# Kernel tuning notes

Measured on AMD Instinct MI355X. Metric: run time of the kernel, lower is better.

Reference implementation:

```python
import jax, jax.numpy as jnp
import numpy as np

EPS = 1e-6

def setup_inputs() -> dict:
    key = jax.random.key(0)
    M, N, D = 6, 4096, 512
    output = jax.random.normal(key, (M, N, D), dtype=jnp.float32)
    return {"output": output}

def reference(output):
    # output: [M, N, D] stacked per-layer features (already flatten(1)'d)
    M, N, _ = output.shape
    # Gram matrices K_i = X_i @ X_i^T with zeroed diagonal: [M, N, N]
    K = jnp.einsum('ind,imd->inm', output, output)
    K = K * (1.0 - jnp.eye(N, dtype=K.dtype))
    # Double centering H@K@H == K - rowmean - colmean + totalmean
    row = jnp.mean(K, axis=2, keepdims=True)
    col = jnp.mean(K, axis=1, keepdims=True)
    tot = jnp.mean(K, axis=(1, 2), keepdims=True)
    Khat = K - row - col + tot
    # Pairwise HSIC(K_i, K_j) = |sum(Khat_i * Khat_j)| : [M, M]
    S = jnp.abs(jnp.einsum('inm,jnm->ij', Khat, Khat))
    diag = jnp.diagonal(S)
    cka = S / jnp.sqrt(diag[:, None] * diag[None, :] + EPS)
    # Original only fills the strict lower triangle
    hsic_matrix = cka * jnp.tril(jnp.ones((M, M), dtype=cka.dtype), k=-1)
    l = jnp.sum(jnp.abs(hsic_matrix))
    hsic_visual = hsic_matrix + hsic_matrix.T + jnp.eye(M, dtype=cka.dtype)
    return (hsic_visual, l)
```

## Files before the change

### kernel.cpp

```cpp
#include <hip/hip_runtime.h>
#include <hip/hip_bf16.h>
#include <stdint.h>


#define NPTS  4096
#define DF    512
#define ML    6
#define NPAIR 21
#define BKB   128
#define NDIAGBLK 60
#define NOFFBLK  240
#define NGEMMBLK (NDIAGBLK + NOFFBLK)
#define NSTATS   192
#define NTAIL    21
#define TILEB (128 * BKB)

typedef float  f32x4 __attribute__((ext_vector_type(4)));
typedef int    i32x4v __attribute__((ext_vector_type(4)));
typedef int    i32x8v __attribute__((ext_vector_type(8)));
typedef unsigned char u8;

__constant__ int c_PI[NPAIR] = {0,0,0,0,0,0, 1,1,1,1,1, 2,2,2,2, 3,3,3, 4,4, 5};
__constant__ int c_PJ[NPAIR] = {0,1,2,3,4,5, 1,2,3,4,5, 2,3,4,5, 3,4,5, 4,5, 5};
__constant__ int c_DIAGP[ML]  = {0, 6, 11, 15, 18, 20};
__constant__ int c_OFFP[15]   = {1,2,3,4,5, 7,8,9,10, 12,13,14, 16,17, 19};
__constant__ int c_TM[10] = {0,0,0,0, 1,1,1, 2,2, 3};
__constant__ int c_TN[10] = {0,1,2,3, 1,2,3, 2,3, 3};

#define OFF_XT8  0u
#define OFF_SP   12582912u
#define OFF_DVP  13369344u
#define OFF_F    14155776u
#define OFF_D    (OFF_F + 1024u)
#define OFF_XS   (OFF_D + 98304u)
#define OFF_DD   (OFF_XS + 98304u)
#define OFF_RD   (OFF_DD + 256u)
#define OFF_T    (OFF_RD + 256u)

#define UNIT_SCALE 127

__device__ __forceinline__ unsigned short f2fp8x2(float a, float b) {
    return (unsigned short)(__builtin_amdgcn_cvt_pk_fp8_f32(a, b, 0, false) & 0xffff);
}

__device__ __forceinline__ void gl2lds16(const void* g, void* l) {
    __builtin_amdgcn_global_load_lds(
        (__attribute__((address_space(1))) void*)g,
        (__attribute__((address_space(3))) void*)l, 16, 0, 0);
}

__device__ __forceinline__ i32x8v frag32(const u8* base, int row, int quad) {
    int sw = row & 7;
    i32x4v lo = *(const i32x4v*)&base[row * BKB + ((2 * quad) ^ sw) * 16];
    i32x4v hi = *(const i32x4v*)&base[row * BKB + ((2 * quad + 1) ^ sw) * 16];
    return __builtin_shufflevector(lo, hi, 0, 1, 2, 3, 4, 5, 6, 7);
}

__device__ __forceinline__ void stage128(const u8* __restrict__ G, u8* L,
                                         int wave, int rl, int g, int k0) {
#pragma unroll
    for (int is = 0; is < 4; ++is) {
        int rbase = is * 32 + wave * 8;
        int r = rbase + rl;
        int gs = g ^ (r & 7);
        gl2lds16(G + (size_t)r * NPTS + k0 + gs * 16, &L[rbase * BKB]);
    }
}

__global__ __launch_bounds__(256) void k_transpose(const float* __restrict__ X,
                                                   u8* __restrict__ Xt8,
                                                   float* __restrict__ sp,
                                                   float* __restrict__ dvp,
                                                   float* __restrict__ F,
                                                   unsigned* __restrict__ cnt,
                                                   float* __restrict__ tbss,
                                                   float* __restrict__ dv,
                                                   float* __restrict__ xs) {
    __shared__ float tT[64][67];
    int nt = blockIdx.x, dt = blockIdx.y, l = blockIdx.z;
    int n0 = nt * 64, d0 = dt * 64;
    int t = threadIdx.x, q = t & 15, r = t >> 4;
    if (dt == 0) {
        int zb = (l << 6) + nt;
        if (t < 64)            dv[zb * 64 + t] = 0.f;
        else if (t < 128)      xs[zb * 64 + (t - 64)] = 0.f;
        if (zb == 0) {
            if (t >= 128 && t < 128 + NPAIR) F[t - 128] = 0.f;
            if (t == 155) *cnt = 0u;
            if (t >= 160 && t < 160 + ML) tbss[t - 160] = 0.f;
        }
    }
    const float4* src = (const float4*)(X + ((size_t)l * NPTS + n0) * DF + d0);
#pragma unroll
    for (int p = 0; p < 4; ++p) {
        int rr = r + 16 * p;
        float4 v = src[(size_t)rr * (DF / 4) + q];
        tT[4 * q + 0][rr] = v.x;
        tT[4 * q + 1][rr] = v.y;
        tT[4 * q + 2][rr] = v.z;
        tT[4 * q + 3][rr] = v.w;
    }
    __syncthreads();
    if (t < 64) {
        float cs = 0.f;
#pragma unroll
        for (int k = 0; k < 64; ++k) {
            int n = (6 * t + k) & 63;
            cs += tT[t][n];
        }
        sp[((l << 6) + nt) * DF + d0 + t] = cs;
    } else if (t < 128) {
        int n = t - 64;
        float rs = 0.f;
#pragma unroll
        for (int d = 0; d < 64; ++d) { float v = tT[d][n]; rs += v * v; }
        dvp[((l << 3) + dt) * NPTS + n0 + n] = rs;
    }
    int dcol = t >> 2, nb = (t & 3) * 16;
    uint4 o;
#pragma unroll
    for (int w2 = 0; w2 < 4; ++w2) {
        int j = nb + w2 * 4;
        unsigned lo = f2fp8x2(tT[dcol][j + 0], tT[dcol][j + 1]);
        unsigned hi = f2fp8x2(tT[dcol][j + 2], tT[dcol][j + 3]);
        ((unsigned*)&o)[w2] = lo | (hi << 16);
    }
    *(uint4*)(Xt8 + ((size_t)(l * DF + d0 + dcol)) * NPTS + n0 + nb) = o;
}

__global__ __launch_bounds__(256, 2) void k_gemm_frob(const u8* __restrict__ Xt8,
                                                      float* __restrict__ F,
                                                      const float* __restrict__ sp,
                                                      const float* __restrict__ dvp,
                                                      float* __restrict__ dv,
                                                      float* __restrict__ xs,
                                                      float* __restrict__ tbss) {
    __shared__ __align__(16) u8 As[2][TILEB];
    __shared__ __align__(16) u8 Bs[2][TILEB];

    int orig = blockIdx.x;
    int b = orig;
    if (orig < NGEMMBLK) {
        int xcd = orig & 7, idx = orig >> 3;
        const int q = NGEMMBLK >> 3, r = NGEMMBLK & 7;
        b = (xcd < r ? xcd * (q + 1) : r * (q + 1) + (xcd - r) * q) + idx;
    }
    int t = threadIdx.x, wave = t >> 6, lane = t & 63;
    int rl = lane >> 3, g = lane & 7;
    int row16 = lane & 15, quad = lane >> 4;

    if (b < NGEMMBLK) {
        const u8* A;
        const u8* B;
        int p;
        float w = 1.0f;
        if (b < NDIAGBLK) {
            int li = b / 10, tt = b % 10;
            p = c_DIAGP[li];
            w = (c_TM[tt] == c_TN[tt]) ? 1.0f : 2.0f;
            A = Xt8 + ((size_t)(li * DF + c_TM[tt] * 128)) * NPTS;
            B = Xt8 + ((size_t)(li * DF + c_TN[tt] * 128)) * NPTS;
        } else {
            int b2 = b - NDIAGBLK, op = b2 >> 4, tile = b2 & 15;
            p = c_OFFP[op];
            A = Xt8 + ((size_t)(c_PI[p] * DF + (tile & 3) * 128)) * NPTS;
            B = Xt8 + ((size_t)(c_PJ[p] * DF + (tile >> 2) * 128)) * NPTS;
        }

        int wr = (wave >> 1) * 64, wc = (wave & 1) * 64;
        f32x4 acc[4][4];
#pragma unroll
        for (int mi = 0; mi < 4; ++mi)
#pragma unroll
            for (int ni = 0; ni < 4; ++ni) acc[mi][ni] = (f32x4)0.0f;

        stage128(A, As[0], wave, rl, g, 0);
        stage128(B, Bs[0], wave, rl, g, 0);
        int cur = 0;
        const int NIT = NPTS / BKB;
        for (int it = 0; it < NIT; ++it) {
            if (it < NIT - 1) {
                int kN = (it + 1) * BKB;
                stage128(A, As[cur ^ 1], wave, rl, g, kN);
                stage128(B, Bs[cur ^ 1], wave, rl, g, kN);
                asm volatile("s_waitcnt vmcnt(8)" ::: "memory");
            } else {
                asm volatile("s_waitcnt vmcnt(0)" ::: "memory");
            }
            __builtin_amdgcn_s_barrier();
            asm volatile("" ::: "memory");
            i32x8v af[4];
#pragma unroll
            for (int mi = 0; mi < 4; ++mi)
                af[mi] = frag32(As[cur], wr + mi * 16 + row16, quad);
#pragma unroll
            for (int ni = 0; ni < 4; ++ni) {
                i32x8v bf = frag32(Bs[cur], wc + ni * 16 + row16, quad);
#pragma unroll
                for (int mi = 0; mi < 4; ++mi)
                    acc[mi][ni] = __builtin_amdgcn_mfma_scale_f32_16x16x128_f8f6f4(
                        af[mi], bf, acc[mi][ni], 0, 0,
                        0, UNIT_SCALE, 0, UNIT_SCALE);
            }
            asm volatile("s_waitcnt lgkmcnt(0)" ::: "memory");
            __builtin_amdgcn_s_barrier();
            asm volatile("" ::: "memory");
            cur ^= 1;
        }

        float local = 0.f;
#pragma unroll
        for (int mi = 0; mi < 4; ++mi)
#pragma unroll
            for (int ni = 0; ni < 4; ++ni)
#pragma unroll
                for (int e = 0; e < 4; ++e)
                    local += acc[mi][ni][e] * acc[mi][ni][e];
        for (int off = 32; off; off >>= 1) local += __shfl_down(local, off);
        __shared__ float wsum[4];
        if (lane == 0) wsum[wave] = local;
        __syncthreads();
        if (t == 0)
            atomicAdd(&F[p], w * (wsum[0] + wsum[1] + wsum[2] + wsum[3]));
    } else {
        int sid = b - NGEMMBLK;
        int l = sid >> 5, rem = sid & 31, dc = rem >> 2, nc = rem & 3;
        int d0 = dc * 64, n0 = nc * 1024;
        float* scratch = (float*)As;
        float* slp = (float*)As + 256;

        int dl = t & 63, part = t >> 6;
        float a = 0.f;
#pragma unroll 4
        for (int k = 0; k < 16; ++k)
            a += sp[((l << 6) + part * 16 + k) * DF + d0 + dl];
        scratch[t] = a;
        __syncthreads();
        if (t < 64)
            slp[t] = scratch[t] + scratch[64 + t] + scratch[128 + t] + scratch[192 + t];
        __syncthreads();
        if (nc == 0 && t == 0) {
            float q2 = 0.f;
#pragma unroll
            for (int d = 0; d < 64; ++d) q2 += slp[d] * slp[d];
            atomicAdd(&tbss[l], q2);
        }
        int n = n0 + t * 4;
        const u8* xb = Xt8 + (size_t)(l * DF + d0) * NPTS + n;
        float a0 = 0, a1 = 0, a2 = 0, a3 = 0;
#pragma unroll 8
        for (int dd = 0; dd < 64; ++dd) {
            unsigned v = *(const unsigned*)(xb + (size_t)dd * NPTS);
            float sv = slp[dd];
            a0 += sv * __builtin_amdgcn_cvt_f32_fp8(v, 0);
            a1 += sv * __builtin_amdgcn_cvt_f32_fp8(v, 1);
            a2 += sv * __builtin_amdgcn_cvt_f32_fp8(v, 2);
            a3 += sv * __builtin_amdgcn_cvt_f32_fp8(v, 3);
        }
        float* xo = xs + l * NPTS + n;
        atomicAdd(&xo[0], a0); atomicAdd(&xo[1], a1);
        atomicAdd(&xo[2], a2); atomicAdd(&xo[3], a3);
        float4 dp = *(const float4*)(dvp + ((l << 3) + dc) * NPTS + n);
        float* dvo = dv + l * NPTS + n;
        atomicAdd(&dvo[0], dp.x); atomicAdd(&dvo[1], dp.y);
        atomicAdd(&dvo[2], dp.z); atomicAdd(&dvo[3], dp.w);
    }
}

__global__ __launch_bounds__(256) void k_tail(const float* __restrict__ dv,
                                              const float* __restrict__ xs,
                                              const float* __restrict__ tbss,
                                              float* __restrict__ F,
                                              float* __restrict__ ddot,
                                              float* __restrict__ rdot,
                                              float* __restrict__ tb,
                                              unsigned* __restrict__ cnt,
                                              float* __restrict__ out) {
    __shared__ float4 red[256];
    __shared__ int lastFlag;
    __shared__ float tbv[ML];
    __shared__ double hs[ML][ML];
    __shared__ float cka[ML][ML];

    int b = blockIdx.x, t = threadIdx.x;

    {
        int p = b, i = c_PI[p], j = c_PJ[p];
        const float invN = 1.0f / (float)NPTS;
        float dd = 0.f, rr = 0.f, sd = 0.f;
        for (int n = t; n < NPTS; n += 256) {
            float di = dv[i * NPTS + n], dj = dv[j * NPTS + n];
            float ri = (xs[i * NPTS + n] - di) * invN;
            float rj = (xs[j * NPTS + n] - dj) * invN;
            dd += di * dj;
            rr += ri * rj;
            sd += di;
        }
        red[t] = make_float4(dd, rr, sd, 0.f);
        __syncthreads();
        for (int h = 128; h > 0; h >>= 1) {
            if (t < h) {
                float4 a = red[t], bb = red[t + h];
                red[t] = make_float4(a.x + bb.x, a.y + bb.y, a.z + bb.z, 0.f);
            }
            __syncthreads();
        }
        if (t == 0) {
            atomicExch(&ddot[p], red[0].x);
            atomicExch(&rdot[p], red[0].y);
            if (i == j)
                atomicExch(&tb[i],
                    (tbss[i] - red[0].z) * (1.0f / ((float)NPTS * (float)NPTS)));
        }
    }

    __syncthreads();
    if (t == 0) {
        __threadfence();
        unsigned old = atomicAdd(cnt, 1u);
        lastFlag = (old == NTAIL - 1);
    }
    __syncthreads();
    if (!lastFlag) return;
    __threadfence();
    if (t < ML) tbv[t] = atomicAdd(&tb[t], 0.0f);
    __syncthreads();
    if (t < NPAIR) {
        int i = c_PI[t], j = c_PJ[t];
        double Fv = (double)atomicAdd(&F[t], 0.0f);
        double dd = (double)atomicAdd(&ddot[t], 0.0f);
        double rd = (double)atomicAdd(&rdot[t], 0.0f);
        double v = Fv - dd - 2.0 * (double)NPTS * rd
                 + (double)NPTS * (double)NPTS * (double)tbv[i] * (double)tbv[j];
        hs[i][j] = v; hs[j][i] = v;
    }
    __syncthreads();
    if (t < ML * ML) {
        int i = t / ML, j = t % ML;
        float v;
        if (i == j) v = 1.0f;
        else v = (float)(fabs(hs[i][j]) / sqrt(hs[i][i] * hs[j][j] + 1e-6));
        cka[i][j] = v;
        out[t] = v;
    }
    __syncthreads();
    if (t == 0) {
        float l = 0.f;
        for (int i = 1; i < ML; ++i)
            for (int j = 0; j < i; ++j) l += cka[i][j];
        out[ML * ML] = l;
    }
}

extern "C" void kernel_launch(void* const* d_in, const int* in_sizes, int n_in,
                              void* d_out, int out_size, void* d_ws, size_t ws_size,
                              hipStream_t stream) {
    (void)in_sizes; (void)n_in; (void)out_size; (void)ws_size;
    const float* X = (const float*)d_in[0];
    float* out = (float*)d_out;
    char* ws = (char*)d_ws;
    u8*    Xt8 = (u8*)(ws + OFF_XT8);
    float* sp  = (float*)(ws + OFF_SP);
    float* dvp = (float*)(ws + OFF_DVP);
    float* F   = (float*)(ws + OFF_F);
    unsigned* cnt = (unsigned*)(ws + OFF_F + 256u);
    float* tbss = (float*)(ws + OFF_F + 512u);
    float* dv  = (float*)(ws + OFF_D);
    float* xs  = (float*)(ws + OFF_XS);
    float* dd  = (float*)(ws + OFF_DD);
    float* rd  = (float*)(ws + OFF_RD);
    float* tb  = (float*)(ws + OFF_T);

    hipLaunchKernelGGL(k_transpose, dim3(64, 8, 6), dim3(256), 0, stream,
                       X, Xt8, sp, dvp, F, cnt, tbss, dv, xs);
    hipLaunchKernelGGL(k_gemm_frob, dim3(NGEMMBLK + NSTATS), dim3(256), 0, stream,
                       Xt8, F, sp, dvp, dv, xs, tbss);
    hipLaunchKernelGGL(k_tail, dim3(NTAIL), dim3(256), 0, stream,
                       dv, xs, tbss, F, dd, rd, tb, cnt, out);
}
```

Before: 130.1 us.

## Use 512-thread blocks with 8 waves per GEMM tile and merge stats blocks

```diff
diff --git a/kernel.cpp b/kernel.cpp
--- a/kernel.cpp
+++ b/kernel.cpp
@@ -11,7 +11,7 @@
 #define NDIAGBLK 60
 #define NOFFBLK  240
 #define NGEMMBLK (NDIAGBLK + NOFFBLK)
-#define NSTATS   192
+#define NSTATS   96
 #define NTAIL    21
 #define TILEB (128 * BKB)
 
@@ -56,11 +56,11 @@
     return __builtin_shufflevector(lo, hi, 0, 1, 2, 3, 4, 5, 6, 7);
 }
 
-__device__ __forceinline__ void stage128(const u8* __restrict__ G, u8* L,
-                                         int wave, int rl, int g, int k0) {
-#pragma unroll
-    for (int is = 0; is < 4; ++is) {
-        int rbase = is * 32 + wave * 8;
+__device__ __forceinline__ void stage128w8(const u8* __restrict__ G, u8* L,
+                                           int wave, int rl, int g, int k0) {
+#pragma unroll
+    for (int is = 0; is < 2; ++is) {
+        int rbase = is * 64 + wave * 8;
         int r = rbase + rl;
         int gs = g ^ (r & 7);
         gl2lds16(G + (size_t)r * NPTS + k0 + gs * 16, &L[rbase * BKB]);
@@ -128,7 +128,7 @@
     *(uint4*)(Xt8 + ((size_t)(l * DF + d0 + dcol)) * NPTS + n0 + nb) = o;
 }
 
-__global__ __launch_bounds__(256, 2) void k_gemm_frob(const u8* __restrict__ Xt8,
+__global__ __launch_bounds__(512, 4) void k_gemm_frob(const u8* __restrict__ Xt8,
                                                       float* __restrict__ F,
                                                       const float* __restrict__ sp,
                                                       const float* __restrict__ dvp,
@@ -167,23 +167,23 @@
             B = Xt8 + ((size_t)(c_PJ[p] * DF + (tile >> 2) * 128)) * NPTS;
         }
 
-        int wr = (wave >> 1) * 64, wc = (wave & 1) * 64;
-        f32x4 acc[4][4];
+        int wr = (wave >> 2) * 64, wc = (wave & 3) * 32;
+        f32x4 acc[4][2];
 #pragma unroll
         for (int mi = 0; mi < 4; ++mi)
 #pragma unroll
-            for (int ni = 0; ni < 4; ++ni) acc[mi][ni] = (f32x4)0.0f;
-
-        stage128(A, As[0], wave, rl, g, 0);
-        stage128(B, Bs[0], wave, rl, g, 0);
+            for (int ni = 0; ni < 2; ++ni) acc[mi][ni] = (f32x4)0.0f;
+
+        stage128w8(A, As[0], wave, rl, g, 0);
+        stage128w8(B, Bs[0], wave, rl, g, 0);
         int cur = 0;
         const int NIT = NPTS / BKB;
         for (int it = 0; it < NIT; ++it) {
             if (it < NIT - 1) {
                 int kN = (it + 1) * BKB;
-                stage128(A, As[cur ^ 1], wave, rl, g, kN);
-                stage128(B, Bs[cur ^ 1], wave, rl, g, kN);
-                asm volatile("s_waitcnt vmcnt(8)" ::: "memory");
+                stage128w8(A, As[cur ^ 1], wave, rl, g, kN);
+                stage128w8(B, Bs[cur ^ 1], wave, rl, g, kN);
+                asm volatile("s_waitcnt vmcnt(4)" ::: "memory");
             } else {
                 asm volatile("s_waitcnt vmcnt(0)" ::: "memory");
             }
@@ -194,7 +194,7 @@
             for (int mi = 0; mi < 4; ++mi)
                 af[mi] = frag32(As[cur], wr + mi * 16 + row16, quad);
 #pragma unroll
-            for (int ni = 0; ni < 4; ++ni) {
+            for (int ni = 0; ni < 2; ++ni) {
                 i32x8v bf = frag32(Bs[cur], wc + ni * 16 + row16, quad);
 #pragma unroll
                 for (int mi = 0; mi < 4; ++mi)
@@ -212,40 +212,45 @@
 #pragma unroll
         for (int mi = 0; mi < 4; ++mi)
 #pragma unroll
-            for (int ni = 0; ni < 4; ++ni)
+            for (int ni = 0; ni < 2; ++ni)
 #pragma unroll
                 for (int e = 0; e < 4; ++e)
                     local += acc[mi][ni][e] * acc[mi][ni][e];
         for (int off = 32; off; off >>= 1) local += __shfl_down(local, off);
-        __shared__ float wsum[4];
+        __shared__ float wsum[8];
         if (lane == 0) wsum[wave] = local;
         __syncthreads();
-        if (t == 0)
-            atomicAdd(&F[p], w * (wsum[0] + wsum[1] + wsum[2] + wsum[3]));
+        if (t == 0) {
+            float s = 0.f;
+#pragma unroll
+            for (int k = 0; k < 8; ++k) s += wsum[k];
+            atomicAdd(&F[p], w * s);
+        }
     } else {
-        int sid = b - NGEMMBLK;
+        int half = t >> 8, tl = t & 255;
+        int sid = (b - NGEMMBLK) * 2 + half;
         int l = sid >> 5, rem = sid & 31, dc = rem >> 2, nc = rem & 3;
         int d0 = dc * 64, n0 = nc * 1024;
-        float* scratch = (float*)As;
-        float* slp = (float*)As + 256;
-
-        int dl = t & 63, part = t >> 6;
+        float* scratch = (float*)As + half * 384;
+        float* slp = scratch + 256;
+
+        int dl = tl & 63, part = tl >> 6;
         float a = 0.f;
 #pragma unroll 4
         for (int k = 0; k < 16; ++k)
             a += sp[((l << 6) + part * 16 + k) * DF + d0 + dl];
-        scratch[t] = a;
+        scratch[tl] = a;
         __syncthreads();
-        if (t < 64)
-            slp[t] = scratch[t] + scratch[64 + t] + scratch[128 + t] + scratch[192 + t];
+        if (tl < 64)
+            slp[tl] = scratch[tl] + scratch[64 + tl] + scratch[128 + tl] + scratch[192 + tl];
         __syncthreads();
-        if (nc == 0 && t == 0) {
+        if (nc == 0 && tl == 0) {
             float q2 = 0.f;
 #pragma unroll
             for (int d = 0; d < 64; ++d) q2 += slp[d] * slp[d];
             atomicAdd(&tbss[l], q2);
         }
-        int n = n0 + t * 4;
+        int n = n0 + tl * 4;
         const u8* xb = Xt8 + (size_t)(l * DF + d0) * NPTS + n;
         float a0 = 0, a1 = 0, a2 = 0, a3 = 0;
 #pragma unroll 8
@@ -373,7 +378,7 @@
 
     hipLaunchKernelGGL(k_transpose, dim3(64, 8, 6), dim3(256), 0, stream,
                        X, Xt8, sp, dvp, F, cnt, tbss, dv, xs);
-    hipLaunchKernelGGL(k_gemm_frob, dim3(NGEMMBLK + NSTATS), dim3(256), 0, stream,
+    hipLaunchKernelGGL(k_gemm_frob, dim3(NGEMMBLK + NSTATS), dim3(512), 0, stream,
                        Xt8, F, sp, dvp, dv, xs, tbss);
     hipLaunchKernelGGL(k_tail, dim3(NTAIL), dim3(256), 0, stream,
                        dv, xs, tbss, F, dd, rd, tb, cnt, out);
```

After: 129.5 us. About the same (-0.5%).
